# Kernel tuning notes

Measured on AMD Instinct MI355X. Metric: run time of the kernel, lower is better.

Reference implementation:

```python
import jax, jax.numpy as jnp
import numpy as np

TAU = 2.0        # args.tau default (spikingjelly LIFNode)
V_TH = 1.0       # v_threshold
V_RESET = 0.0    # v_reset (hard reset)
ALPHA = 2.0      # ATan surrogate alpha

@jax.custom_vjp
def atan_spike(x):
    # Heaviside spike with ATan surrogate gradient (spikingjelly surrogate.ATan)
    return (x >= 0.0).astype(x.dtype)

def _atan_fwd(x):
    return atan_spike(x), x

def _atan_bwd(x, g):
    sg = (ALPHA / 2.0) / (1.0 + (jnp.pi / 2.0 * ALPHA * x) ** 2)
    return (g * sg,)

atan_spike.defvjp(_atan_fwd, _atan_bwd)

def setup_inputs() -> dict:
    key = jax.random.key(0)
    k1, k2, k3 = jax.random.split(key, 3)
    T, B, IN, OUT, NC = 16, 512, 3072, 2048, 10
    x_seq = jax.random.normal(k1, (T, B, IN), dtype=jnp.float32)
    # xavier-uniform-like scale: sqrt(2/(fan_in+fan_out))
    fc_w = jax.random.normal(k2, (OUT, IN), dtype=jnp.float32) * np.sqrt(2.0 / (IN + OUT)).astype(np.float32)
    fc_b = jnp.zeros((OUT,), jnp.float32)
    aux_w = jax.random.normal(k3, (NC, OUT), dtype=jnp.float32) * np.sqrt(2.0 / (OUT + NC)).astype(np.float32)
    aux_b = jnp.zeros((NC,), jnp.float32)
    return {"x_seq": x_seq, "fc_w": fc_w, "fc_b": fc_b, "aux_w": aux_w, "aux_b": aux_b}

def reference(x_seq, fc_w, fc_b, aux_w, aux_b):
    # fc over all timesteps: [T,B,in] @ [out,in]^T -> [T,B,out]
    cur_seq = jnp.einsum('tbi,oi->tbo', x_seq, fc_w) + fc_b

    def step(v, c):
        # LIF charge: v += (x - (v - v_reset)) / tau
        v = v + (c - (v - V_RESET)) / TAU
        s = atan_spike(v - V_TH)
        s_d = jax.lax.stop_gradient(s)  # detach_reset=True
        v = (1.0 - s_d) * v + s_d * V_RESET  # hard reset
        return v, s

    v0 = jnp.full(cur_seq.shape[1:], V_RESET, cur_seq.dtype)  # reset_net -> v = v_reset
    _, spk_seq = jax.lax.scan(step, v0, cur_seq)  # spk_seq: [T,B,out]
    count = spk_seq.sum(axis=0)                    # [B,out]
    logits = count @ aux_w.T + aux_b               # aux_head local logits [B,10]
    return spk_seq, count, logits
```

## Files before the change

### kernel.cpp

```cpp
#include <hip/hip_runtime.h>
#include <hip/hip_bf16.h>
#include <stdint.h>

#define T_   16
#define B_   512
#define IN_  3072
#define OUT_ 2048
#define NC_  10
#define M_   (T_ * B_)

#define BM 128
#define BN 128

#define SPK_SZ ((size_t)T_ * B_ * OUT_)
#define CNT_SZ ((size_t)B_ * OUT_)

#define TOL 4e-4
#define MAXFLAG (B_ * OUT_)

#define BK2   32
#define NCH2  (IN_ / BK2)
#define TILE_US 8192
#define APAN (M_ / BM)
#define BPAN (OUT_ / BN)

typedef __attribute__((ext_vector_type(8))) short s16x8;
typedef __attribute__((ext_vector_type(4))) float f32x4;

__device__ unsigned int g_ctr;
__device__ unsigned int g_list[MAXFLAG];

__global__ void zero_ctr() { if (threadIdx.x == 0) g_ctr = 0; }

__device__ __forceinline__ unsigned short f2bf(float f) {
    __bf16 h = (__bf16)f;
    return *(unsigned short*)&h;
}
__device__ __forceinline__ float bf2f(unsigned short u) {
    union { unsigned int i; float f; } c; c.i = ((unsigned int)u) << 16; return c.f;
}
__device__ __forceinline__ int swz8(int r, int g) {
    return r * 64 + ((g ^ (r & 7)) << 3);
}
__device__ __forceinline__ int swz(int r, int g) {
    return r * 64 + ((g ^ (r & 7)) << 3);
}

__device__ __forceinline__ void gload_lds16(const void* g, void* l) {
    __builtin_amdgcn_global_load_lds(
        (const __attribute__((address_space(1))) unsigned int*)g,
        (__attribute__((address_space(3))) unsigned int*)l, 16, 0, 0);
}

__global__ __launch_bounds__(256)
void prep(const float* __restrict__ src, unsigned short* __restrict__ dst)
{
    const int id = blockIdx.x * 256 + threadIdx.x;
    const int gk = id & 3;
    const int r  = (id >> 2) & 127;
    const int ch = (id >> 9) % NCH2;
    const int pa = id / (NCH2 * 512);
    const int m  = pa * 128 + r;
    const int k  = ch * BK2 + gk * 8;

    float f[8];
    *(float4*)&f[0] = *(const float4*)(src + (size_t)m * IN_ + k);
    *(float4*)&f[4] = *(const float4*)(src + (size_t)m * IN_ + k + 4);
    s16x8 hi, lo;
#pragma unroll
    for (int j = 0; j < 8; ++j) {
        unsigned short hb = f2bf(f[j]);
        hi[j] = (short)hb;
        lo[j] = (short)f2bf(f[j] - bf2f(hb));
    }
    unsigned short* tb = dst + ((size_t)pa * NCH2 + ch) * TILE_US;
    *(s16x8*)&tb[swz8(r, gk)]     = hi;
    *(s16x8*)&tb[swz8(r, gk + 4)] = lo;
}

__global__ __launch_bounds__(256, 3)
void gemm_lds(const unsigned short* __restrict__ Adig,
              const unsigned short* __restrict__ Bdig,
              float* __restrict__ cur)
{
    __shared__ __align__(16) unsigned short Ash[TILE_US];
    __shared__ __align__(16) unsigned short Bsh[TILE_US];

    const int tid = threadIdx.x;
    const int l   = tid & 63;
    const int wv  = tid >> 6;
    const int wm  = (wv >> 1) * 64;
    const int wn  = (wv & 1) * 64;

    const int lin = blockIdx.x + blockIdx.y * gridDim.x;
    const int s   = (lin & 7) * 128 + (lin >> 3);
    const int pm  = s % APAN;
    const int pn  = s / APAN;
    const int m0  = pm * BM;
    const int n0  = pn * BN;

    f32x4 acc[4][4];
#pragma unroll
    for (int i = 0; i < 4; ++i)
#pragma unroll
        for (int j = 0; j < 4; ++j) acc[i][j] = (f32x4)0.0f;

    const int lp = l & 15;
    const int lq = l >> 4;
    const int l8 = l * 8;

    const unsigned short* Abase = Adig + (size_t)pm * NCH2 * TILE_US;
    const unsigned short* Bbase = Bdig + (size_t)pn * NCH2 * TILE_US;

    for (int ch = 0; ch < NCH2; ++ch) {
        __syncthreads();
        if (wv < 2) {
            const unsigned short* sA = Abase + (size_t)ch * TILE_US + wv * 4096;
            unsigned short* dA = Ash + wv * 4096;
#pragma unroll
            for (int i = 0; i < 8; ++i)
                gload_lds16(sA + i * 512 + l8, dA + i * 512);
        } else {
            const unsigned short* sB = Bbase + (size_t)ch * TILE_US + (wv - 2) * 4096;
            unsigned short* dB = Bsh + (wv - 2) * 4096;
#pragma unroll
            for (int i = 0; i < 8; ++i)
                gload_lds16(sB + i * 512 + l8, dB + i * 512);
        }
        __syncthreads();

        s16x8 a1f[4], a2f[4], b1f[4], b2f[4];
#pragma unroll
        for (int i = 0; i < 4; ++i) {
            const int ra = wm + i * 16 + lp;
            a1f[i] = *(const s16x8*)&Ash[swz8(ra, lq)];
            a2f[i] = *(const s16x8*)&Ash[swz8(ra, lq + 4)];
            const int rb = wn + i * 16 + lp;
            b1f[i] = *(const s16x8*)&Bsh[swz8(rb, lq)];
            b2f[i] = *(const s16x8*)&Bsh[swz8(rb, lq + 4)];
        }
#pragma unroll
        for (int i = 0; i < 4; ++i)
#pragma unroll
            for (int j = 0; j < 4; ++j) {
                acc[i][j] = __builtin_amdgcn_mfma_f32_16x16x32_bf16(
                    a1f[i], b1f[j], acc[i][j], 0, 0, 0);
                acc[i][j] = __builtin_amdgcn_mfma_f32_16x16x32_bf16(
                    a2f[i], b1f[j], acc[i][j], 0, 0, 0);
                acc[i][j] = __builtin_amdgcn_mfma_f32_16x16x32_bf16(
                    a1f[i], b2f[j], acc[i][j], 0, 0, 0);
            }
    }

    const int crow = lq * 4, ccol = lp;
#pragma unroll
    for (int i = 0; i < 4; ++i)
#pragma unroll
        for (int j = 0; j < 4; ++j) {
            const size_t mbase = (size_t)(m0 + wm + i * 16 + crow);
            const int o = n0 + wn + j * 16 + ccol;
#pragma unroll
            for (int reg = 0; reg < 4; ++reg)
                cur[(mbase + reg) * OUT_ + o] = acc[i][j][reg];
        }
}

__global__ __launch_bounds__(256, 2)
void gemm_split(const float* __restrict__ x, const float* __restrict__ w,
                float* __restrict__ cur)
{
    __shared__ __align__(16) unsigned short A1[BM * 64];
    __shared__ __align__(16) unsigned short A2[BM * 64];
    __shared__ __align__(16) unsigned short B1[BN * 64];
    __shared__ __align__(16) unsigned short B2[BN * 64];

    const int tid = threadIdx.x;
    const int l   = tid & 63;
    const int wv  = tid >> 6;
    const int wm  = (wv >> 1) * 64;
    const int wn  = (wv & 1) * 64;
    const int m0  = blockIdx.x * BM;
    const int n0  = blockIdx.y * BN;

    const int r = tid >> 1;
    const int h = tid & 1;
    const float* xa = x + (size_t)(m0 + r) * IN_ + h * 32;
    const float* wa = w + (size_t)(n0 + r) * IN_ + h * 32;

    f32x4 acc[4][4];
#pragma unroll
    for (int i = 0; i < 4; ++i)
#pragma unroll
        for (int j = 0; j < 4; ++j) acc[i][j] = (f32x4)0.0f;

    const int lp = l & 15;
    const int lq = l >> 4;

    for (int ch = 0; ch < 48; ++ch) {
        const int k0 = ch * 64;
        __syncthreads();
        float fx[32], fw[32];
#pragma unroll
        for (int i = 0; i < 8; ++i)
            *(float4*)&fx[4 * i] = *(const float4*)(xa + k0 + 4 * i);
#pragma unroll
        for (int i = 0; i < 8; ++i)
            *(float4*)&fw[4 * i] = *(const float4*)(wa + k0 + 4 * i);

#pragma unroll
        for (int q = 0; q < 4; ++q) {
            s16x8 vh, vl, uh, ul;
#pragma unroll
            for (int j = 0; j < 8; ++j) {
                float f = fx[8 * q + j];
                unsigned short hb = f2bf(f);
                vh[j] = (short)hb;
                vl[j] = (short)f2bf(f - bf2f(hb));
                float g = fw[8 * q + j];
                unsigned short gb = f2bf(g);
                uh[j] = (short)gb;
                ul[j] = (short)f2bf(g - bf2f(gb));
            }
            const int gg = h * 4 + q;
            *(s16x8*)&A1[swz(r, gg)] = vh;
            *(s16x8*)&A2[swz(r, gg)] = vl;
            *(s16x8*)&B1[swz(r, gg)] = uh;
            *(s16x8*)&B2[swz(r, gg)] = ul;
        }
        __syncthreads();

#pragma unroll
        for (int kk = 0; kk < 2; ++kk) {
            const int gb = kk * 4 + lq;
            s16x8 a1f[4], a2f[4], b1f[4], b2f[4];
#pragma unroll
            for (int i = 0; i < 4; ++i) {
                const int ra = wm + i * 16 + lp;
                a1f[i] = *(const s16x8*)&A1[swz(ra, gb)];
                a2f[i] = *(const s16x8*)&A2[swz(ra, gb)];
                const int rb = wn + i * 16 + lp;
                b1f[i] = *(const s16x8*)&B1[swz(rb, gb)];
                b2f[i] = *(const s16x8*)&B2[swz(rb, gb)];
            }
#pragma unroll
            for (int i = 0; i < 4; ++i)
#pragma unroll
                for (int j = 0; j < 4; ++j) {
                    acc[i][j] = __builtin_amdgcn_mfma_f32_16x16x32_bf16(
                        a1f[i], b1f[j], acc[i][j], 0, 0, 0);
                    acc[i][j] = __builtin_amdgcn_mfma_f32_16x16x32_bf16(
                        a2f[i], b1f[j], acc[i][j], 0, 0, 0);
                    acc[i][j] = __builtin_amdgcn_mfma_f32_16x16x32_bf16(
                        a1f[i], b2f[j], acc[i][j], 0, 0, 0);
                }
        }
    }

    const int crow = lq * 4, ccol = lp;
#pragma unroll
    for (int i = 0; i < 4; ++i)
#pragma unroll
        for (int j = 0; j < 4; ++j) {
            const size_t mbase = (size_t)(m0 + wm + i * 16 + crow);
            const int o = n0 + wn + j * 16 + ccol;
#pragma unroll
            for (int reg = 0; reg < 4; ++reg)
                cur[(mbase + reg) * OUT_ + o] = acc[i][j][reg];
        }
}

__global__ __launch_bounds__(256)
void lif_pass(const float* __restrict__ fcb, float* __restrict__ out)
{
    const int idx = blockIdx.x * 256 + threadIdx.x;
    const int o = idx & (OUT_ - 1);
    const double bias = (double)fcb[o];
    double v = 0.0; int cnt = 0; bool fl = false;
#pragma unroll
    for (int t = 0; t < T_; ++t) {
        const size_t p = (size_t)t * CNT_SZ + idx;
        double c = (double)out[p] + bias;
        v = v + (c - v) * 0.5;
        double d = v - 1.0;
        bool s = d >= 0.0;
        if (fabs(d) < TOL) fl = true;
        out[p] = s ? 1.0f : 0.0f;
        cnt += s ? 1 : 0;
        if (s) v = 0.0;
    }
    out[SPK_SZ + idx] = (float)cnt;
    if (fl) {
        unsigned int pI = atomicAdd(&g_ctr, 1u);
        g_list[pI] = (unsigned int)idx;
    }
}

__global__ void fixup(const float* __restrict__ x, const float* __restrict__ w,
                      const float* __restrict__ fcb, float* __restrict__ out)
{
    int nf = (int)g_ctr; if (nf > MAXFLAG) nf = MAXFLAG;
    const int lane = threadIdx.x & 63;
    const int wid  = (blockIdx.x * blockDim.x + threadIdx.x) >> 6;
    const int nw   = (gridDim.x * blockDim.x) >> 6;

    for (int i = wid; i < nf; i += nw) {
        unsigned int e = g_list[i];
        int b = (int)(e >> 11), o = (int)(e & (OUT_ - 1));
        double part[T_];
#pragma unroll
        for (int t = 0; t < T_; ++t) part[t] = 0.0;
        const float* wrow = w + (size_t)o * IN_;
        for (int k = lane; k < IN_; k += 64) {
            double wvv = (double)wrow[k];
#pragma unroll
            for (int t = 0; t < T_; ++t)
                part[t] = fma((double)x[((size_t)t * B_ + b) * IN_ + k], wvv, part[t]);
        }
#pragma unroll
        for (int t = 0; t < T_; ++t)
#pragma unroll
            for (int off = 32; off > 0; off >>= 1)
                part[t] += __shfl_xor(part[t], off, 64);
        if (lane == 0) {
            double bias = (double)fcb[o];
            double v = 0.0; int cnt = 0;
#pragma unroll
            for (int t = 0; t < T_; ++t) {
                double c = part[t] + bias;
                v = v + (c - v) * 0.5;
                bool s = (v - 1.0) >= 0.0;
                out[(size_t)t * CNT_SZ + (size_t)b * OUT_ + o] = s ? 1.0f : 0.0f;
                cnt += s ? 1 : 0;
                if (s) v = 0.0;
            }
            out[SPK_SZ + (size_t)b * OUT_ + o] = (float)cnt;
        }
    }
}

__global__ void aux_logits(const float* __restrict__ cnt,
                           const float* __restrict__ aw,
                           const float* __restrict__ ab,
                           float* __restrict__ lg)
{
    const int b = blockIdx.x;
    const int lane = threadIdx.x;
    double p0=0,p1=0,p2=0,p3=0,p4=0,p5=0,p6=0,p7=0,p8=0,p9=0;
    for (int o = lane; o < OUT_; o += 64) {
        double c = (double)cnt[(size_t)b * OUT_ + o];
        p0 = fma(c, (double)aw[0 * OUT_ + o], p0);
        p1 = fma(c, (double)aw[1 * OUT_ + o], p1);
        p2 = fma(c, (double)aw[2 * OUT_ + o], p2);
        p3 = fma(c, (double)aw[3 * OUT_ + o], p3);
        p4 = fma(c, (double)aw[4 * OUT_ + o], p4);
        p5 = fma(c, (double)aw[5 * OUT_ + o], p5);
        p6 = fma(c, (double)aw[6 * OUT_ + o], p6);
        p7 = fma(c, (double)aw[7 * OUT_ + o], p7);
        p8 = fma(c, (double)aw[8 * OUT_ + o], p8);
        p9 = fma(c, (double)aw[9 * OUT_ + o], p9);
    }
#pragma unroll
    for (int off = 32; off > 0; off >>= 1) {
        p0 += __shfl_xor(p0, off, 64); p1 += __shfl_xor(p1, off, 64);
        p2 += __shfl_xor(p2, off, 64); p3 += __shfl_xor(p3, off, 64);
        p4 += __shfl_xor(p4, off, 64); p5 += __shfl_xor(p5, off, 64);
        p6 += __shfl_xor(p6, off, 64); p7 += __shfl_xor(p7, off, 64);
        p8 += __shfl_xor(p8, off, 64); p9 += __shfl_xor(p9, off, 64);
    }
    if (lane == 0) {
        double pv[NC_] = {p0,p1,p2,p3,p4,p5,p6,p7,p8,p9};
#pragma unroll
        for (int c = 0; c < NC_; ++c)
            lg[(size_t)b * NC_ + c] = (float)(pv[c] + (double)ab[c]);
    }
}

extern "C" void kernel_launch(void* const* d_in, const int* in_sizes, int n_in,
                              void* d_out, int out_size, void* d_ws, size_t ws_size,
                              hipStream_t stream)
{
    (void)in_sizes; (void)n_in; (void)out_size;
    const float* x   = (const float*)d_in[0];
    const float* w   = (const float*)d_in[1];
    const float* fcb = (const float*)d_in[2];
    const float* aw  = (const float*)d_in[3];
    const float* ab  = (const float*)d_in[4];
    float* out = (float*)d_out;

    zero_ctr<<<dim3(1), dim3(64), 0, stream>>>();

    const size_t needA = (size_t)APAN * NCH2 * TILE_US * 2;
    const size_t needB = (size_t)BPAN * NCH2 * TILE_US * 2;

    if (ws_size >= needA + needB) {
        unsigned short* Adig = (unsigned short*)d_ws;
        unsigned short* Bdig = Adig + (size_t)APAN * NCH2 * TILE_US;
        prep<<<dim3(APAN * NCH2 * 512 / 256), dim3(256), 0, stream>>>(x, Adig);
        prep<<<dim3(BPAN * NCH2 * 512 / 256), dim3(256), 0, stream>>>(w, Bdig);
        gemm_lds<<<dim3(APAN, BPAN), dim3(256), 0, stream>>>(Adig, Bdig, out);
    } else {
        gemm_split<<<dim3(M_ / BM, OUT_ / BN), dim3(256), 0, stream>>>(x, w, out);
    }

    lif_pass<<<dim3(CNT_SZ / 256), dim3(256), 0, stream>>>(fcb, out);

    fixup<<<dim3(512), dim3(256), 0, stream>>>(x, w, fcb, out);

    aux_logits<<<dim3(B_), dim3(64), 0, stream>>>(
        out + SPK_SZ, aw, ab, out + SPK_SZ + CNT_SZ);
}
```

Measured before the change: 408.4 us.

## Double-buffer LDS tiles in GEMM, fuse prep launches, remap XCD tile order

The GEMM main loop now uses two LDS buffers per operand. The next K-chunk's global-to-LDS loads are issued while the MFMAs consume the current one, and one barrier per iteration replaces two. The two prep launches and the counter-zeroing launch are merged into one kernel. The grid becomes 1D with a new block-to-tile mapping that groups M-panels per XCD for L2 reuse. Doubling LDS drops the occupancy hint from 3 to 2 blocks per CU.

```diff
diff --git a/kernel.cpp b/kernel.cpp
--- a/kernel.cpp
+++ b/kernel.cpp
@@ -24,6 +24,9 @@
 #define APAN (M_ / BM)
 #define BPAN (OUT_ / BN)
 
+#define A_PREP_BLOCKS (APAN * NCH2 * 2)
+#define B_PREP_BLOCKS (BPAN * NCH2 * 2)
+
 typedef __attribute__((ext_vector_type(8))) short s16x8;
 typedef __attribute__((ext_vector_type(4))) float f32x4;
 
@@ -40,9 +43,6 @@
     union { unsigned int i; float f; } c; c.i = ((unsigned int)u) << 16; return c.f;
 }
 __device__ __forceinline__ int swz8(int r, int g) {
-    return r * 64 + ((g ^ (r & 7)) << 3);
-}
-__device__ __forceinline__ int swz(int r, int g) {
     return r * 64 + ((g ^ (r & 7)) << 3);
 }
 
@@ -53,9 +53,17 @@
 }
 
 __global__ __launch_bounds__(256)
-void prep(const float* __restrict__ src, unsigned short* __restrict__ dst)
-{
-    const int id = blockIdx.x * 256 + threadIdx.x;
+void prep2(const float* __restrict__ x, const float* __restrict__ w,
+           unsigned short* __restrict__ Adig, unsigned short* __restrict__ Bdig)
+{
+    if (blockIdx.x == 0 && threadIdx.x == 0) g_ctr = 0;
+
+    const float* src; unsigned short* dst; int id;
+    if (blockIdx.x < A_PREP_BLOCKS) {
+        src = x; dst = Adig; id = blockIdx.x * 256 + threadIdx.x;
+    } else {
+        src = w; dst = Bdig; id = (blockIdx.x - A_PREP_BLOCKS) * 256 + threadIdx.x;
+    }
     const int gk = id & 3;
     const int r  = (id >> 2) & 127;
     const int ch = (id >> 9) % NCH2;
@@ -78,13 +86,13 @@
     *(s16x8*)&tb[swz8(r, gk + 4)] = lo;
 }
 
-__global__ __launch_bounds__(256, 3)
+__global__ __launch_bounds__(256, 2)
 void gemm_lds(const unsigned short* __restrict__ Adig,
               const unsigned short* __restrict__ Bdig,
               float* __restrict__ cur)
 {
-    __shared__ __align__(16) unsigned short Ash[TILE_US];
-    __shared__ __align__(16) unsigned short Bsh[TILE_US];
+    __shared__ __align__(16) unsigned short Ash[2][TILE_US];
+    __shared__ __align__(16) unsigned short Bsh[2][TILE_US];
 
     const int tid = threadIdx.x;
     const int l   = tid & 63;
@@ -92,10 +100,11 @@
     const int wm  = (wv >> 1) * 64;
     const int wn  = (wv & 1) * 64;
 
-    const int lin = blockIdx.x + blockIdx.y * gridDim.x;
-    const int s   = (lin & 7) * 128 + (lin >> 3);
-    const int pm  = s % APAN;
-    const int pn  = s / APAN;
+    const int lin = blockIdx.x;
+    const int xcd = lin & 7;
+    const int jj  = lin >> 3;
+    const int pm  = xcd * 8 + (jj & 7);
+    const int pn  = jj >> 3;
     const int m0  = pm * BM;
     const int n0  = pn * BN;
 
@@ -112,32 +121,38 @@
     const unsigned short* Abase = Adig + (size_t)pm * NCH2 * TILE_US;
     const unsigned short* Bbase = Bdig + (size_t)pn * NCH2 * TILE_US;
 
-    for (int ch = 0; ch < NCH2; ++ch) {
-        __syncthreads();
+    auto stage = [&](int ch, int d) {
         if (wv < 2) {
             const unsigned short* sA = Abase + (size_t)ch * TILE_US + wv * 4096;
-            unsigned short* dA = Ash + wv * 4096;
+            unsigned short* dA = &Ash[d][wv * 4096];
 #pragma unroll
             for (int i = 0; i < 8; ++i)
                 gload_lds16(sA + i * 512 + l8, dA + i * 512);
         } else {
             const unsigned short* sB = Bbase + (size_t)ch * TILE_US + (wv - 2) * 4096;
-            unsigned short* dB = Bsh + (wv - 2) * 4096;
+            unsigned short* dB = &Bsh[d][(wv - 2) * 4096];
 #pragma unroll
             for (int i = 0; i < 8; ++i)
                 gload_lds16(sB + i * 512 + l8, dB + i * 512);
         }
-        __syncthreads();
+    };
+
+    stage(0, 0);
+    __syncthreads();
+
+    for (int ch = 0; ch < NCH2; ++ch) {
+        const int d = ch & 1;
+        if (ch + 1 < NCH2) stage(ch + 1, d ^ 1);
 
         s16x8 a1f[4], a2f[4], b1f[4], b2f[4];
 #pragma unroll
         for (int i = 0; i < 4; ++i) {
             const int ra = wm + i * 16 + lp;
-            a1f[i] = *(const s16x8*)&Ash[swz8(ra, lq)];
-            a2f[i] = *(const s16x8*)&Ash[swz8(ra, lq + 4)];
+            a1f[i] = *(const s16x8*)&Ash[d][swz8(ra, lq)];
+            a2f[i] = *(const s16x8*)&Ash[d][swz8(ra, lq + 4)];
             const int rb = wn + i * 16 + lp;
-            b1f[i] = *(const s16x8*)&Bsh[swz8(rb, lq)];
-            b2f[i] = *(const s16x8*)&Bsh[swz8(rb, lq + 4)];
+            b1f[i] = *(const s16x8*)&Bsh[d][swz8(rb, lq)];
+            b2f[i] = *(const s16x8*)&Bsh[d][swz8(rb, lq + 4)];
         }
 #pragma unroll
         for (int i = 0; i < 4; ++i)
@@ -150,6 +165,7 @@
                 acc[i][j] = __builtin_amdgcn_mfma_f32_16x16x32_bf16(
                     a1f[i], b2f[j], acc[i][j], 0, 0, 0);
             }
+        __syncthreads();
     }
 
     const int crow = lq * 4, ccol = lp;
@@ -222,10 +238,10 @@
                 ul[j] = (short)f2bf(g - bf2f(gb));
             }
             const int gg = h * 4 + q;
-            *(s16x8*)&A1[swz(r, gg)] = vh;
-            *(s16x8*)&A2[swz(r, gg)] = vl;
-            *(s16x8*)&B1[swz(r, gg)] = uh;
-            *(s16x8*)&B2[swz(r, gg)] = ul;
+            *(s16x8*)&A1[swz8(r, gg)] = vh;
+            *(s16x8*)&A2[swz8(r, gg)] = vl;
+            *(s16x8*)&B1[swz8(r, gg)] = uh;
+            *(s16x8*)&B2[swz8(r, gg)] = ul;
         }
         __syncthreads();
 
@@ -236,11 +252,11 @@
 #pragma unroll
             for (int i = 0; i < 4; ++i) {
                 const int ra = wm + i * 16 + lp;
-                a1f[i] = *(const s16x8*)&A1[swz(ra, gb)];
-                a2f[i] = *(const s16x8*)&A2[swz(ra, gb)];
+                a1f[i] = *(const s16x8*)&A1[swz8(ra, gb)];
+                a2f[i] = *(const s16x8*)&A2[swz8(ra, gb)];
                 const int rb = wn + i * 16 + lp;
-                b1f[i] = *(const s16x8*)&B1[swz(rb, gb)];
-                b2f[i] = *(const s16x8*)&B2[swz(rb, gb)];
+                b1f[i] = *(const s16x8*)&B1[swz8(rb, gb)];
+                b2f[i] = *(const s16x8*)&B2[swz8(rb, gb)];
             }
 #pragma unroll
             for (int i = 0; i < 4; ++i)
@@ -387,18 +403,17 @@
     const float* ab  = (const float*)d_in[4];
     float* out = (float*)d_out;
 
-    zero_ctr<<<dim3(1), dim3(64), 0, stream>>>();
-
     const size_t needA = (size_t)APAN * NCH2 * TILE_US * 2;
     const size_t needB = (size_t)BPAN * NCH2 * TILE_US * 2;
 
     if (ws_size >= needA + needB) {
         unsigned short* Adig = (unsigned short*)d_ws;
         unsigned short* Bdig = Adig + (size_t)APAN * NCH2 * TILE_US;
-        prep<<<dim3(APAN * NCH2 * 512 / 256), dim3(256), 0, stream>>>(x, Adig);
-        prep<<<dim3(BPAN * NCH2 * 512 / 256), dim3(256), 0, stream>>>(w, Bdig);
-        gemm_lds<<<dim3(APAN, BPAN), dim3(256), 0, stream>>>(Adig, Bdig, out);
+        prep2<<<dim3(A_PREP_BLOCKS + B_PREP_BLOCKS), dim3(256), 0, stream>>>(
+            x, w, Adig, Bdig);
+        gemm_lds<<<dim3(APAN * BPAN), dim3(256), 0, stream>>>(Adig, Bdig, out);
     } else {
+        zero_ctr<<<dim3(1), dim3(64), 0, stream>>>();
         gemm_split<<<dim3(M_ / BM, OUT_ / BN), dim3(256), 0, stream>>>(x, w, out);
     }
 
```

Measured after the change: 401.6 us. Within noise of the previous version (-1.7%).
